# Performance work log

Hardware: AMD Instinct MI355X
Metric: run time of the kernel (lower is better)

## Reference

```python
import jax, jax.numpy as jnp
import numpy as np

N = 10000      # nodes
E = 100000     # edges
D = 768        # hidden = heads * head_dim
H = 4          # heads
C = D // H     # 192 per-head channels
EDIM = 16      # edge feature dim
NREL = 10      # num relations
L = 3          # num TransformerConv layers


def setup_inputs() -> dict:
    key = jax.random.key(0)
    ks = jax.random.split(key, 16)
    s = 0.02
    x = jax.random.normal(ks[0], (N, D), jnp.float32)
    edge_index = jax.random.randint(ks[1], (2, E), 0, N, jnp.int32)
    rel = jax.random.randint(ks[2], (E,), 0, NREL).astype(jnp.float32)
    w = jax.random.uniform(ks[3], (E,), jnp.float32)
    edge_attr = jnp.stack([rel, w], axis=1)  # [E, 2]: (relation_id, weight)
    rel_emb = jax.random.normal(ks[4], (NREL, EDIM - 1), jnp.float32) * s
    W_edge = jax.random.normal(ks[5], (EDIM, EDIM), jnp.float32) * s
    b_edge = jnp.zeros((EDIM,), jnp.float32)
    Wk = jax.random.normal(ks[6], (L, D, D), jnp.float32) * s
    bk = jnp.zeros((L, D), jnp.float32)
    Wq = jax.random.normal(ks[7], (L, D, D), jnp.float32) * s
    bq = jnp.zeros((L, D), jnp.float32)
    Wv = jax.random.normal(ks[8], (L, D, D), jnp.float32) * s
    bv = jnp.zeros((L, D), jnp.float32)
    We = jax.random.normal(ks[9], (L, EDIM, D), jnp.float32) * s   # lin_edge, no bias (PyG)
    Wskip = jax.random.normal(ks[10], (L, D, D), jnp.float32) * s  # root/skip linear
    bskip = jnp.zeros((L, D), jnp.float32)
    ln_g = jnp.ones((D,), jnp.float32)
    ln_b = jnp.zeros((D,), jnp.float32)
    return dict(x=x, edge_attr=edge_attr, edge_index=edge_index, rel_emb=rel_emb,
                W_edge=W_edge, b_edge=b_edge, Wk=Wk, bk=bk, Wq=Wq, bq=bq,
                Wv=Wv, bv=bv, We=We, Wskip=Wskip, bskip=bskip, ln_g=ln_g, ln_b=ln_b)


def reference(x, edge_attr, edge_index, rel_emb, W_edge, b_edge,
              Wk, bk, Wq, bq, Wv, bv, We, Wskip, bskip, ln_g, ln_b):
    src, dst = edge_index[0], edge_index[1]
    # _process_edge_features: embed relation id, concat weight, project
    rel_ids = jnp.clip(jax.lax.stop_gradient(edge_attr[:, 0]).astype(jnp.int32), 0, NREL - 1)
    ef = jnp.concatenate([rel_emb[rel_ids], edge_attr[:, 1:2]], axis=-1) @ W_edge + b_edge  # [E,16]
    scale = 1.0 / np.sqrt(C)
    h = x  # input_proj is Identity (input_dim == hidden_dim)
    for l in range(L):
        q = (h @ Wq[l] + bq[l]).reshape(N, H, C)
        k = (h @ Wk[l] + bk[l]).reshape(N, H, C)
        v = (h @ Wv[l] + bv[l]).reshape(N, H, C)
        e = (ef @ We[l]).reshape(E, H, C)           # per-edge embedding
        kj = k[src] + e                              # [E,H,C]
        alpha = jnp.einsum('ehc,ehc->eh', q[dst], kj) * scale  # [E,H]
        # scatter-softmax over incoming edges of each destination node
        m = jax.ops.segment_max(jax.lax.stop_gradient(alpha), dst, num_segments=N)
        a = jnp.exp(alpha - m[dst])
        denom = jax.ops.segment_sum(a, dst, num_segments=N)
        a = a / (denom[dst] + 1e-16)
        msg = (v[src] + e) * a[..., None]            # [E,H,C]
        out = jax.ops.segment_sum(msg.reshape(E, H * C), dst, num_segments=N)
        h = out + h @ Wskip[l] + bskip[l]            # root_weight skip connection
        if l < L - 1:
            h = jax.nn.gelu(h, approximate=False)    # dropout: eval mode -> identity
    mu = jnp.mean(h, axis=-1, keepdims=True)
    var = jnp.mean((h - mu) ** 2, axis=-1, keepdims=True)
    h = (h - mu) / jnp.sqrt(var + 1e-5) * ln_g + ln_b
    return jnp.mean(h, axis=0)  # global_mean_pool over single graph -> [D]
```

## Files before the change

### kernel.cpp

```cpp
#include <hip/hip_runtime.h>
#include <hip/hip_bf16.h>
#include <math.h>
#include <stdint.h>

#define NN 10000
#define EE 100000
#define DD 768
#define HH 4
#define CC 192
#define EDIM 16
#define NREL 10
#define MP 10240
#define NQ2 3200
#define NB 3136
#define SCALE 0.07216878364870322f

using short8  = __attribute__((ext_vector_type(8))) short;
using floatx4 = __attribute__((ext_vector_type(4))) float;


__device__ __forceinline__ float b2f(short u) {
    union { unsigned int i; float f; } t;
    t.i = ((unsigned int)(unsigned short)u) << 16;
    return t.f;
}

__device__ __forceinline__ short f2b(float f) {
    __hip_bfloat16 h = __float2bfloat16(f);
    short r;
    __builtin_memcpy(&r, &h, 2);
    return r;
}

__device__ __forceinline__ __hip_bfloat16 rd_any(const void* p, long long j, int bf) {
    if (bf) return ((const __hip_bfloat16*)p)[j];
    return __float2bfloat16(((const float*)p)[j]);
}

__device__ __forceinline__ void gload16(const __hip_bfloat16* g, __hip_bfloat16* l) {
    __builtin_amdgcn_global_load_lds(
        (const __attribute__((address_space(1))) unsigned int*)g,
        (__attribute__((address_space(3))) unsigned int*)l, 16, 0, 0);
}

__global__ __launch_bounds__(256) void detect_zero(const void* edge_attr,
                                                   int* flag, int* counts,
                                                   float* accum) {
    int i = blockIdx.x * 256 + threadIdx.x;
    if (i < NN) counts[i] = 0;
    if (i < DD) accum[i] = 0.0f;
    if (blockIdx.x == 0 && threadIdx.x < 64) {
        const unsigned short* p = (const unsigned short*)edge_attr;
        int nz = (p[4 * threadIdx.x] != 0) ? 1 : 0;
        unsigned long long m = __ballot(nz);
        if (threadIdx.x == 0) *flag = (__popcll(m) > 8) ? 1 : 0;
    }
}


__global__ __launch_bounds__(256) void cvt_big(
    const void* x, const void* We, const int* flag,
    __hip_bfloat16* hb, __hip_bfloat16* Web) {
    long long i = (long long)blockIdx.x * 256 + threadIdx.x;
    int bf = *flag;
    const long long NX = (long long)NN * DD;
    const long long NE2 = 3LL * EDIM * DD;
    if (i < NX) { hb[i] = rd_any(x, i, bf); return; } i -= NX;
    if (i < NE2) { Web[i] = rd_any(We, i, bf); return; } i -= NE2;
    if (i < (long long)(MP - NN) * DD) hb[(long long)NN * DD + i] = __float2bfloat16(0.0f);
}

__global__ __launch_bounds__(256) void cvt_small(
    const void* ea, const void* rel, const void* Wed, const void* bed,
    const void* bk, const void* bq, const void* bv, const void* bs,
    const void* lg, const void* lb, const int* flag,
    __hip_bfloat16* eab, __hip_bfloat16* relb, __hip_bfloat16* Wedb,
    __hip_bfloat16* bedb, __hip_bfloat16* ballb, __hip_bfloat16* lgb,
    __hip_bfloat16* lbb) {
    long long i = (long long)blockIdx.x * 256 + threadIdx.x;
    int bf = *flag;
    if (i < 2LL * EE) { eab[i] = rd_any(ea, i, bf); return; } i -= 2LL * EE;
    if (i < NREL * (EDIM - 1)) { relb[i] = rd_any(rel, i, bf); return; } i -= NREL * (EDIM - 1);
    if (i < EDIM * EDIM) { Wedb[i] = rd_any(Wed, i, bf); return; } i -= EDIM * EDIM;
    if (i < EDIM) { bedb[i] = rd_any(bed, i, bf); return; } i -= EDIM;
    if (i < 3 * NB) {
        int l = (int)(i / NB), c = (int)(i % NB);
        const void* src; long long off; int outc;
        if (c < 768)       { src = bq; off = (long long)l * DD + c; outc = c; }
        else if (c < 1536) { int xx = c - 768;  src = bk;
                             off = (long long)l * DD + xx;
                             outc = 768 + (xx / 6) * 12 + xx % 6; }
        else if (c < 2304) { int xx = c - 1536; src = bv;
                             off = (long long)l * DD + xx;
                             outc = 768 + (xx / 6) * 12 + 6 + xx % 6; }
        else if (c < 3072) { src = bs; off = (long long)l * DD + (c - 2304); outc = c; }
        else { ballb[l * NB + c] = __float2bfloat16(0.0f); return; }
        ballb[l * NB + outc] = rd_any(src, off, bf); return;
    } i -= 3 * NB;
    if (i < DD) { lgb[i] = rd_any(lg, i, bf); return; } i -= DD;
    if (i < DD) { lbb[i] = rd_any(lb, i, bf); return; }
}

__global__ __launch_bounds__(256) void wt_all(
    const void* Wq, const void* Wk, const void* Wv, const void* Ws,
    const int* flag, __hip_bfloat16* Wt3) {
    __shared__ __hip_bfloat16 tile[32][33];
    int mm = blockIdx.y;
    int l = mm >> 2, m = mm & 3;
    const void* src = (m == 0) ? Wq : (m == 1) ? Wk : (m == 2) ? Wv : Ws;
    int bx = blockIdx.x;
    int tr = bx / 24, tc = bx % 24;
    int k0 = tr * 32, c0 = tc * 32;
    int t = threadIdx.x;
    int rr = t >> 5, cc = t & 31;
    int bf = *flag;
    long long base = (long long)l * DD * DD;
#pragma unroll
    for (int p = 0; p < 4; p++)
        tile[p * 8 + rr][cc] =
            rd_any(src, base + (long long)(k0 + p * 8 + rr) * DD + c0 + cc, bf);
    __syncthreads();
    __hip_bfloat16* base_l = Wt3 + (size_t)l * NB * DD;
#pragma unroll
    for (int p = 0; p < 4; p++) {
        int xcol = c0 + p * 8 + rr;
        int row;
        if (m == 1)      row = 768 + (xcol / 6) * 12 + xcol % 6;
        else if (m == 2) row = 768 + (xcol / 6) * 12 + 6 + xcol % 6;
        else             row = m * 768 + xcol;
        base_l[(size_t)row * DD + k0 + cc] = tile[cc][p * 8 + rr];
    }
}

__global__ __launch_bounds__(256) void mq_kernel(
    const void* Wq, const void* bq, const int* flag,
    const __hip_bfloat16* __restrict__ Web, __hip_bfloat16* __restrict__ Wt3,
    __hip_bfloat16* __restrict__ ballb) {
    __shared__ float WeS[16][193];
    const int lh = blockIdx.y, l = lh >> 2, hh = lh & 3;
    const int t = threadIdx.x;
    const int bf = *flag;
    for (int i = t; i < 16 * 192; i += 256) {
        int j = i / 192, c = i % 192;
        WeS[j][c] = (float)Web[(size_t)l * EDIM * DD + (size_t)j * DD + hh * CC + c];
    }
    __syncthreads();
    const int k = blockIdx.x * 64 + (t >> 2);
    const int j0 = (t & 3) * 4;
    float s0 = 0.f, s1 = 0.f, s2 = 0.f, s3 = 0.f;
    if (bf) {
        const short8* qp = (const short8*)((const __hip_bfloat16*)Wq +
            ((size_t)l * DD + k) * DD + hh * CC);
#pragma unroll 4
        for (int ch = 0; ch < 24; ch++) {
            short8 v = qp[ch];
#pragma unroll
            for (int u = 0; u < 8; u++) {
                float w = b2f(v[u]);
                int c = ch * 8 + u;
                s0 += w * WeS[j0 + 0][c]; s1 += w * WeS[j0 + 1][c];
                s2 += w * WeS[j0 + 2][c]; s3 += w * WeS[j0 + 3][c];
            }
        }
    } else {
        const float4* qp = (const float4*)((const float*)Wq +
            ((size_t)l * DD + k) * DD + hh * CC);
#pragma unroll 4
        for (int ch = 0; ch < 48; ch++) {
            float4 v = qp[ch];
            float wv[4] = {v.x, v.y, v.z, v.w};
#pragma unroll
            for (int u = 0; u < 4; u++) {
                float w = wv[u];
                int c = ch * 4 + u;
                s0 += w * WeS[j0 + 0][c]; s1 += w * WeS[j0 + 1][c];
                s2 += w * WeS[j0 + 2][c]; s3 += w * WeS[j0 + 3][c];
            }
        }
    }
    const size_t base = (size_t)l * NB * DD;
    const int row = 3072 + hh * 16 + j0;
    Wt3[base + (size_t)(row + 0) * DD + k] = __float2bfloat16(s0);
    Wt3[base + (size_t)(row + 1) * DD + k] = __float2bfloat16(s1);
    Wt3[base + (size_t)(row + 2) * DD + k] = __float2bfloat16(s2);
    Wt3[base + (size_t)(row + 3) * DD + k] = __float2bfloat16(s3);
    if (blockIdx.x == 0 && t < 4) {
        float b0 = 0.f, b1 = 0.f, b2 = 0.f, b3 = 0.f;
        for (int c = 0; c < CC; c++) {
            float w = (float)rd_any(bq, (long long)l * DD + hh * CC + c, bf);
            b0 += w * WeS[j0 + 0][c]; b1 += w * WeS[j0 + 1][c];
            b2 += w * WeS[j0 + 2][c]; b3 += w * WeS[j0 + 3][c];
        }
        ballb[l * NB + 3072 + hh * 16 + j0 + 0] = __float2bfloat16(b0);
        ballb[l * NB + 3072 + hh * 16 + j0 + 1] = __float2bfloat16(b1);
        ballb[l * NB + 3072 + hh * 16 + j0 + 2] = __float2bfloat16(b2);
        ballb[l * NB + 3072 + hh * 16 + j0 + 3] = __float2bfloat16(b3);
    }
}


__global__ __launch_bounds__(256) void count_kernel(const int* ei, int* counts) {
    int e = blockIdx.x * 256 + threadIdx.x;
    if (e < EE) atomicAdd(&counts[ei[EE + e]], 1);
}

__global__ __launch_bounds__(256) void scan_kernel(const int* counts, int* rowptr,
                                                   int* cursor) {
    __shared__ int buf[NN];
    __shared__ int sdata[256];
    int t = threadIdx.x;
    for (int j = t; j < NN; j += 256) buf[j] = counts[j];
    __syncthreads();
    int base = t * 40;
    int cnt = (base < NN) ? min(40, NN - base) : 0;
    int s = 0;
    for (int i = 0; i < cnt; i++) s += buf[base + i];
    sdata[t] = s;
    __syncthreads();
    for (int off = 1; off < 256; off <<= 1) {
        int add = (t >= off) ? sdata[t - off] : 0;
        __syncthreads();
        sdata[t] += add;
        __syncthreads();
    }
    int run = sdata[t] - s;
    for (int i = 0; i < cnt; i++) {
        int tmp = buf[base + i];
        buf[base + i] = run;
        run += tmp;
    }
    __syncthreads();
    for (int j = t; j < NN; j += 256) {
        int v = buf[j];
        cursor[j] = v;
        rowptr[j] = v;
    }
    if (t == 0) rowptr[NN] = EE;
}

__global__ __launch_bounds__(256) void fill_kernel(const int* ei, int* cursor,
                                                   int* eids, int* esrc) {
    int e = blockIdx.x * 256 + threadIdx.x;
    if (e < EE) {
        int d = ei[EE + e];
        int pos = atomicAdd(&cursor[d], 1);
        eids[pos] = e;
        esrc[pos] = ei[e];
    }
}


__global__ __launch_bounds__(256) void ef_kernel(
    const int* __restrict__ eids,
    const __hip_bfloat16* __restrict__ eab, const __hip_bfloat16* __restrict__ relb,
    const __hip_bfloat16* __restrict__ Wedb, const __hip_bfloat16* __restrict__ bedb,
    __hip_bfloat16* __restrict__ efb) {
    int idx = blockIdx.x * 256 + threadIdx.x;
    if (idx >= EE * EDIM) return;
    int p = idx >> 4, j = idx & 15;
    int e = eids[p];
    int rid = (int)((float)eab[e * 2 + 0]);
    rid = min(max(rid, 0), NREL - 1);
    float w = (float)eab[e * 2 + 1];
    float s = (float)bedb[j];
#pragma unroll
    for (int i = 0; i < 15; i++)
        s += (float)relb[rid * 15 + i] * (float)Wedb[i * EDIM + j];
    s += w * (float)Wedb[15 * EDIM + j];
    efb[idx] = __float2bfloat16(s);
}


__device__ __forceinline__ void stage_half(const __hip_bfloat16* g, int row0, int ktile,
                                           char* ldsdst, int tid) {
#pragma unroll
    for (int j = 0; j < 2; ++j) {
        int c = j * 512 + tid;
        int row = c >> 3;
        int sch = (c & 7) ^ (row & 7);
        gload16(g + (size_t)(row0 + row) * DD + ktile * 64 + sch * 8,
                (__hip_bfloat16*)(ldsdst + c * 16));
    }
}

#define MF16(va, vb, cc) cc = __builtin_amdgcn_mfma_f32_16x16x32_bf16(va, vb, cc, 0, 0, 0)
#define BAR() __builtin_amdgcn_s_barrier()
#define WLG() asm volatile("s_waitcnt lgkmcnt(0)" ::: "memory")
#define WVM(N) asm volatile("s_waitcnt vmcnt(" #N ")" ::: "memory")
#define SB() __builtin_amdgcn_sched_barrier(0)
#define LDS8(off) (*(const short8*)(smem + (off)))

__global__ __launch_bounds__(512) void gemm256(
    const __hip_bfloat16* __restrict__ A, const __hip_bfloat16* __restrict__ Bt,
    const __hip_bfloat16* __restrict__ bias, __hip_bfloat16* __restrict__ C) {
    __shared__ __align__(16) char smem[131072];
    const int bid = (int)blockIdx.x;
    const int tid = threadIdx.x;
    const int wid = tid >> 6, lane = tid & 63;
    const int quad = lane >> 4, l15 = lane & 15;

    if (bid < 160) {
        const int m0q = bid * 64;
        const __hip_bfloat16* Bq = Bt + (size_t)3072 * DD;
        const int xq0 = (quad ^ (l15 & 7)) * 16;
        const int xq1 = ((quad + 4) ^ (l15 & 7)) * 16;
        floatx4 qacc[4] = {};
        for (int kt = 0; kt < 12; ++kt) {
#pragma unroll
            for (int j = 0; j < 2; ++j) {
                int c = j * 512 + tid;
                int hf = c >> 9;
                int cc = c & 511;
                int row = cc >> 3;
                int sch = (cc & 7) ^ (row & 7);
                const __hip_bfloat16* src = hf
                    ? (Bq + (size_t)row * DD + kt * 64 + sch * 8)
                    : (A + (size_t)(m0q + row) * DD + kt * 64 + sch * 8);
                gload16(src, (__hip_bfloat16*)(smem + c * 16));
            }
            asm volatile("s_waitcnt vmcnt(0)" ::: "memory");
            BAR();
            if (wid < 4) {
                short8 a0 = LDS8((wid * 16 + l15) * 128 + xq0);
                short8 a1 = LDS8((wid * 16 + l15) * 128 + xq1);
#pragma unroll
                for (int nt = 0; nt < 4; ++nt) {
                    short8 b0 = LDS8(8192 + (nt * 16 + l15) * 128 + xq0);
                    short8 b1 = LDS8(8192 + (nt * 16 + l15) * 128 + xq1);
                    MF16(a0, b0, qacc[nt]);
                    MF16(a1, b1, qacc[nt]);
                }
            }
            WLG();
            BAR();
        }
        if (wid < 4) {
#pragma unroll
            for (int nt = 0; nt < 4; ++nt) {
                float bb = (float)bias[3072 + nt * 16 + l15];
#pragma unroll
                for (int r = 0; r < 4; ++r) {
                    int row = m0q + wid * 16 + quad * 4 + r;
                    if (row < NN)
                        C[(size_t)row * NQ2 + 3072 + nt * 16 + l15] =
                            __float2bfloat16(qacc[nt][r] + bb);
                }
            }
        }
        return;
    }

    const int mbid = bid - 160;
    const int wm = wid >> 2, wn = wid & 3;
    const int swz = (mbid & 7) * 60 + (mbid >> 3);
    const int m0 = (swz / 12) * 256;
    const int n0 = (swz % 12) * 256;

    const int xa0 = (quad ^ (l15 & 7)) * 16;
    const int xa1 = ((quad + 4) ^ (l15 & 7)) * 16;
    const int aRow = (wm * 128 + l15) * 128;
    const int bRow = 32768 + (wn * 64 + l15) * 128;

    floatx4 acc[8][4] = {};
    short8 a[4][2], bA[2][2], bB[2][2];

    stage_half(A, m0, 0, smem + 0, tid);
    stage_half(A, m0 + 128, 0, smem + 16384, tid);
    stage_half(Bt, n0, 0, smem + 32768, tid);
    stage_half(Bt, n0 + 128, 0, smem + 49152, tid);
    stage_half(Bt, n0, 1, smem + 98304, tid);
    stage_half(Bt, n0 + 128, 1, smem + 114688, tid);
    WVM(4);
    BAR();

#pragma unroll 1
    for (int it = 0; it < 6; ++it) {
        const int kA = 2 * it + 1;
        const int kB = (it < 5) ? 2 * it + 2 : 0;
        const int kC = (it < 5) ? 2 * it + 3 : 1;
        stage_half(A, m0, kA, smem + 65536, tid);
        stage_half(A, m0 + 128, kA, smem + 81920, tid);
#pragma unroll
        for (int mt = 0; mt < 4; ++mt) {
            a[mt][0] = LDS8(aRow + mt * 2048 + xa0);
            a[mt][1] = LDS8(aRow + mt * 2048 + xa1);
        }
#pragma unroll
        for (int nt = 0; nt < 2; ++nt) {
            bA[nt][0] = LDS8(bRow + nt * 2048 + xa0);
            bA[nt][1] = LDS8(bRow + nt * 2048 + xa1);
            bB[nt][0] = LDS8(bRow + (nt + 2) * 2048 + xa0);
            bB[nt][1] = LDS8(bRow + (nt + 2) * 2048 + xa1);
        }
        SB(); BAR(); WLG(); SB();
        __builtin_amdgcn_s_setprio(1);
#pragma unroll
        for (int mt = 0; mt < 4; ++mt)
#pragma unroll
            for (int nt = 0; nt < 2; ++nt) {
                MF16(a[mt][0], bA[nt][0], acc[mt][nt]);
                MF16(a[mt][1], bA[nt][1], acc[mt][nt]);
                MF16(a[mt][0], bB[nt][0], acc[mt][nt + 2]);
                MF16(a[mt][1], bB[nt][1], acc[mt][nt + 2]);
            }
        __builtin_amdgcn_s_setprio(0);
        stage_half(Bt, n0, kB, smem + 32768, tid);
        stage_half(Bt, n0 + 128, kB, smem + 49152, tid);
#pragma unroll
        for (int mt = 0; mt < 4; ++mt) {
            a[mt][0] = LDS8(aRow + (mt + 4) * 2048 + xa0);
            a[mt][1] = LDS8(aRow + (mt + 4) * 2048 + xa1);
        }
        WVM(4);
        SB(); BAR(); WLG(); SB();
        __builtin_amdgcn_s_setprio(1);
#pragma unroll
        for (int mt = 0; mt < 4; ++mt)
#pragma unroll
            for (int nt = 0; nt < 2; ++nt) {
                MF16(a[mt][0], bB[nt][0], acc[mt + 4][nt + 2]);
                MF16(a[mt][1], bB[nt][1], acc[mt + 4][nt + 2]);
                MF16(a[mt][0], bA[nt][0], acc[mt + 4][nt]);
                MF16(a[mt][1], bA[nt][1], acc[mt + 4][nt]);
            }
        __builtin_amdgcn_s_setprio(0);
        stage_half(A, m0, kB, smem + 0, tid);
        stage_half(A, m0 + 128, kB, smem + 16384, tid);
#pragma unroll
        for (int mt = 0; mt < 4; ++mt) {
            a[mt][0] = LDS8(65536 + aRow + mt * 2048 + xa0);
            a[mt][1] = LDS8(65536 + aRow + mt * 2048 + xa1);
        }
#pragma unroll
        for (int nt = 0; nt < 2; ++nt) {
            bA[nt][0] = LDS8(65536 + bRow + nt * 2048 + xa0);
            bA[nt][1] = LDS8(65536 + bRow + nt * 2048 + xa1);
            bB[nt][0] = LDS8(65536 + bRow + (nt + 2) * 2048 + xa0);
            bB[nt][1] = LDS8(65536 + bRow + (nt + 2) * 2048 + xa1);
        }
        SB(); BAR(); WLG(); SB();
        __builtin_amdgcn_s_setprio(1);
#pragma unroll
        for (int mt = 0; mt < 4; ++mt)
#pragma unroll
            for (int nt = 0; nt < 2; ++nt) {
                MF16(a[mt][0], bA[nt][0], acc[mt][nt]);
                MF16(a[mt][1], bA[nt][1], acc[mt][nt]);
                MF16(a[mt][0], bB[nt][0], acc[mt][nt + 2]);
                MF16(a[mt][1], bB[nt][1], acc[mt][nt + 2]);
            }
        __builtin_amdgcn_s_setprio(0);
        stage_half(Bt, n0, kC, smem + 98304, tid);
        stage_half(Bt, n0 + 128, kC, smem + 114688, tid);
#pragma unroll
        for (int mt = 0; mt < 4; ++mt) {
            a[mt][0] = LDS8(65536 + aRow + (mt + 4) * 2048 + xa0);
            a[mt][1] = LDS8(65536 + aRow + (mt + 4) * 2048 + xa1);
        }
        WVM(4);
        SB(); BAR(); WLG(); SB();
        __builtin_amdgcn_s_setprio(1);
#pragma unroll
        for (int mt = 0; mt < 4; ++mt)
#pragma unroll
            for (int nt = 0; nt < 2; ++nt) {
                MF16(a[mt][0], bB[nt][0], acc[mt + 4][nt + 2]);
                MF16(a[mt][1], bB[nt][1], acc[mt + 4][nt + 2]);
                MF16(a[mt][0], bA[nt][0], acc[mt + 4][nt]);
                MF16(a[mt][1], bA[nt][1], acc[mt + 4][nt]);
            }
        __builtin_amdgcn_s_setprio(0);
    }

    asm volatile("s_waitcnt vmcnt(0)" ::: "memory");
    BAR();
    {
        short* stg = (short*)smem + wid * 1152;
        float bv[4];
#pragma unroll
        for (int nt = 0; nt < 4; ++nt)
            bv[nt] = (float)bias[n0 + wn * 64 + nt * 16 + l15];
        const int rdo = (lane >> 2) * 68 + (lane & 3) * 16;
        const int grow0 = m0 + wm * 128 + (lane >> 2);
        const int gcol = n0 + wn * 64 + (lane & 3) * 16;
#pragma unroll
        for (int mt = 0; mt < 8; ++mt) {
#pragma unroll
            for (int nt = 0; nt < 4; ++nt)
#pragma unroll
                for (int r = 0; r < 4; ++r)
                    stg[(quad * 4 + r) * 68 + nt * 16 + l15] =
                        f2b(acc[mt][nt][r] + bv[nt]);
            asm volatile("s_waitcnt lgkmcnt(0)" ::: "memory");
            short8 v0 = *(const short8*)(stg + rdo);
            short8 v1 = *(const short8*)(stg + rdo + 8);
            int grow = grow0 + mt * 16;
            if (grow < NN) {
                short8* dp = (short8*)(C + (size_t)grow * NQ2 + gcol);
                dp[0] = v0; dp[1] = v1;
            }
            asm volatile("s_waitcnt lgkmcnt(0)" ::: "memory");
        }
    }
}


__global__ __launch_bounds__(256) void node_attn(
    const int* __restrict__ rowptr, const int* __restrict__ esrc,
    const __hip_bfloat16* __restrict__ qkvs, const __hip_bfloat16* __restrict__ efb,
    const __hip_bfloat16* __restrict__ Wel, __hip_bfloat16* __restrict__ hb,
    int do_gelu) {
    const int wv = threadIdx.x >> 6, lane = threadIdx.x & 63;
    const int n = blockIdx.x * 2 + (wv >> 1);
    const int half = wv & 1;
    const int cb = half * 384 + lane * 6;
    const int g = half * 64 + lane;
    const int kvoff = 768 + g * 12;
    const int sj = lane & 15;
    const int hsel = lane & 32;
    const float qe_gate = ((lane & 16) == 0) ? 1.0f : 0.0f;
    const int s0 = rowptr[n], s1 = rowptr[n + 1];
    const short* qk = (const short*)qkvs;
    float q[6];
    {
        const short2* qp = (const short2*)(qk + (size_t)n * NQ2 + cb);
        short2 a = qp[0], b = qp[1], c = qp[2];
        q[0] = b2f(a.x) * SCALE; q[1] = b2f(a.y) * SCALE; q[2] = b2f(b.x) * SCALE;
        q[3] = b2f(b.y) * SCALE; q[4] = b2f(c.x) * SCALE; q[5] = b2f(c.y) * SCALE;
    }
    const float qe_l = b2f(qk[(size_t)n * NQ2 + 3072 + (half * 2 + (lane >> 5)) * 16 + sj])
                       * SCALE * qe_gate;
    float m = -INFINITY, lsum = 0.f, sacc = 0.f;
    float acc[6] = {};
    short4 kvA = {0,0,0,0}, kvB = {0,0,0,0}, kvC = {0,0,0,0};
    float efv = 0.f;
    if (s0 < s1) {
        const short4* kv = (const short4*)(qk + (size_t)esrc[s0] * NQ2 + kvoff);
        kvA = kv[0]; kvB = kv[1]; kvC = kv[2];
        efv = b2f(((const short*)efb)[(size_t)s0 * 16 + sj]);
    }
    for (int p = s0; p < s1; p++) {
        short4 nA = kvA, nB = kvB, nC = kvC;
        float nefv = efv;
        if (p + 1 < s1) {
            const short4* kv = (const short4*)(qk + (size_t)esrc[p + 1] * NQ2 + kvoff);
            nA = kv[0]; nB = kv[1]; nC = kv[2];
            nefv = b2f(((const short*)efb)[(size_t)(p + 1) * 16 + sj]);
        }
        float part = qe_l * efv;
        part += q[0] * b2f(kvA.x) + q[1] * b2f(kvA.y) + q[2] * b2f(kvA.z);
        part += q[3] * b2f(kvA.w) + q[4] * b2f(kvB.x) + q[5] * b2f(kvB.y);
        part += __shfl_xor(part, 1); part += __shfl_xor(part, 2);
        part += __shfl_xor(part, 4); part += __shfl_xor(part, 8);
        part += __shfl_xor(part, 16);
        if (part > m + 8.0f) {
            float sc = __expf(m - part);
            m = part;
            lsum *= sc; sacc *= sc;
#pragma unroll
            for (int i = 0; i < 6; i++) acc[i] *= sc;
        }
        float w = __expf(part - m);
        lsum += w;
        sacc += w * efv;
        acc[0] += w * b2f(kvB.z); acc[1] += w * b2f(kvB.w);
        acc[2] += w * b2f(kvC.x); acc[3] += w * b2f(kvC.y);
        acc[4] += w * b2f(kvC.z); acc[5] += w * b2f(kvC.w);
        kvA = nA; kvB = nB; kvC = nC; efv = nefv;
    }
    float inv = 1.0f / (lsum + 1e-16f);
#pragma unroll
    for (int i = 0; i < 6; i++) acc[i] *= inv;
    float sS = sacc * inv;
    {
        const short2* sp = (const short2*)(qk + (size_t)n * NQ2 + 2304 + cb);
        short2 a = sp[0], b = sp[1], c = sp[2];
        acc[0] += b2f(a.x); acc[1] += b2f(a.y); acc[2] += b2f(b.x);
        acc[3] += b2f(b.y); acc[4] += b2f(c.x); acc[5] += b2f(c.y);
    }
#pragma unroll
    for (int j = 0; j < 16; j++) {
        float sv = __shfl(sS, hsel + j);
        const short2* wp = (const short2*)(Wel + (size_t)j * DD + cb);
        short2 a = wp[0], b = wp[1], c = wp[2];
        acc[0] += sv * b2f(a.x); acc[1] += sv * b2f(a.y); acc[2] += sv * b2f(b.x);
        acc[3] += sv * b2f(b.y); acc[4] += sv * b2f(c.x); acc[5] += sv * b2f(c.y);
    }
    if (do_gelu) {
#pragma unroll
        for (int i = 0; i < 6; i++)
            acc[i] = 0.5f * acc[i] * (1.0f + erff(acc[i] * 0.70710678118654752f));
    }
    short2 o0, o1, o2;
    o0.x = f2b(acc[0]); o0.y = f2b(acc[1]);
    o1.x = f2b(acc[2]); o1.y = f2b(acc[3]);
    o2.x = f2b(acc[4]); o2.y = f2b(acc[5]);
    short2* hp = (short2*)(hb + (size_t)n * DD + cb);
    hp[0] = o0; hp[1] = o1; hp[2] = o2;
}


__global__ __launch_bounds__(256) void ln_pool(
    const __hip_bfloat16* __restrict__ hb, const __hip_bfloat16* __restrict__ g,
    const __hip_bfloat16* __restrict__ b, float* __restrict__ accum) {
    __shared__ float sbuf[4][768];
    int grp = blockIdx.x, t = threadIdx.x;
    int wid = t >> 6, lane = t & 63;
    float gv[12], bv[12], acc[12];
#pragma unroll
    for (int i = 0; i < 12; i++) {
        gv[i] = (float)g[lane + i * 64];
        bv[i] = (float)b[lane + i * 64];
        acc[i] = 0.f;
    }
    for (int r = wid; r < 25; r += 4) {
        const __hip_bfloat16* row = hb + (size_t)(grp * 25 + r) * DD;
        float x[12];
        float s = 0.f, q = 0.f;
#pragma unroll
        for (int i = 0; i < 12; i++) {
            x[i] = (float)row[lane + i * 64];
            s += x[i]; q += x[i] * x[i];
        }
#pragma unroll
        for (int m = 32; m > 0; m >>= 1) {
            s += __shfl_xor(s, m); q += __shfl_xor(q, m);
        }
        float mu = s * (1.0f / 768.0f);
        float ms = q * (1.0f / 768.0f);
        float inv = 1.0f / sqrtf(ms - mu * mu + 1e-5f);
#pragma unroll
        for (int i = 0; i < 12; i++)
            acc[i] += (x[i] - mu) * inv * gv[i] + bv[i];
    }
#pragma unroll
    for (int i = 0; i < 12; i++) sbuf[wid][lane + i * 64] = acc[i];
    __syncthreads();
#pragma unroll
    for (int j = 0; j < 3; j++) {
        int col = t + j * 256;
        atomicAdd(&accum[col],
                  sbuf[0][col] + sbuf[1][col] + sbuf[2][col] + sbuf[3][col]);
    }
}

__global__ __launch_bounds__(256) void pool_final(
    const float* __restrict__ accum, void* __restrict__ out,
    const int* __restrict__ flag) {
    int dd = blockIdx.x * 256 + threadIdx.x;
    if (dd >= DD) return;
    float s = accum[dd] * (1.0f / 10000.0f);
    if (*flag) ((__hip_bfloat16*)out)[dd] = __float2bfloat16(s);
    else ((float*)out)[dd] = s;
}


extern "C" void kernel_launch(void* const* d_in, const int* in_sizes, int n_in,
                              void* d_out, int out_size, void* d_ws, size_t ws_size,
                              hipStream_t stream) {
    const void* x         = d_in[0];
    const void* edge_attr = d_in[1];
    const int*  ei        = (const int*)d_in[2];
    const void* rel_emb   = d_in[3];
    const void* W_edge    = d_in[4];
    const void* b_edge    = d_in[5];
    const void* Wk        = d_in[6];
    const void* bk        = d_in[7];
    const void* Wq        = d_in[8];
    const void* bq        = d_in[9];
    const void* Wv        = d_in[10];
    const void* bv        = d_in[11];
    const void* We        = d_in[12];
    const void* Wskip     = d_in[13];
    const void* bskip     = d_in[14];
    const void* ln_g      = d_in[15];
    const void* ln_b      = d_in[16];

    char* ws = (char*)d_ws;
    int*   flag    = (int*)(ws + 0);
    int*   counts  = (int*)(ws + 256);
    int*   rowptr  = (int*)(ws + 40448);
    int*   cursor  = (int*)(ws + 80640);
    int*   eids    = (int*)(ws + 120832);
    int*   esrc    = (int*)(ws + 520960);
    __hip_bfloat16* efb = (__hip_bfloat16*)(ws + 920960);
    float* accum   = (float*)(ws + 4120960);
    __hip_bfloat16* eab   = (__hip_bfloat16*)(ws + 5349760);
    __hip_bfloat16* relb  = (__hip_bfloat16*)(ws + 5749760);
    __hip_bfloat16* Wedb  = (__hip_bfloat16*)(ws + 5750144);
    __hip_bfloat16* bedb  = (__hip_bfloat16*)(ws + 5750656);
    __hip_bfloat16* ballb = (__hip_bfloat16*)(ws + 5750784);
    __hip_bfloat16* lngb  = (__hip_bfloat16*)(ws + 5770752);
    __hip_bfloat16* lnbb  = (__hip_bfloat16*)(ws + 5772288);
    __hip_bfloat16* Web   = (__hip_bfloat16*)(ws + 5773824);
    __hip_bfloat16* hb    = (__hip_bfloat16*)(ws + 5847552);
    __hip_bfloat16* Wt3   = (__hip_bfloat16*)(ws + 21576192);
    __hip_bfloat16* qkvs  = (__hip_bfloat16*)(ws + 36911616);

    dim3 blk(256);

    detect_zero<<<dim3(40), blk, 0, stream>>>(edge_attr, flag, counts, accum);

    {
        long long tot = (long long)NN * DD + 3LL * EDIM * DD + (long long)(MP - NN) * DD;
        cvt_big<<<dim3((unsigned)((tot + 255) / 256)), blk, 0, stream>>>(x, We, flag, hb, Web);
    }
    {
        long long tot = 2LL * EE + NREL * (EDIM - 1) + EDIM * EDIM + EDIM
                        + 3LL * NB + 2LL * DD;
        cvt_small<<<dim3((unsigned)((tot + 255) / 256)), blk, 0, stream>>>(
            edge_attr, rel_emb, W_edge, b_edge, bk, bq, bv, bskip, ln_g, ln_b,
            flag, eab, relb, Wedb, bedb, ballb, lngb, lnbb);
    }
    wt_all<<<dim3(576, 12), blk, 0, stream>>>(Wq, Wk, Wv, Wskip, flag, Wt3);
    mq_kernel<<<dim3(12, 12), blk, 0, stream>>>(Wq, bq, flag, Web, Wt3, ballb);

    count_kernel<<<dim3((EE + 255) / 256), blk, 0, stream>>>(ei, counts);
    scan_kernel<<<dim3(1), blk, 0, stream>>>(counts, rowptr, cursor);
    fill_kernel<<<dim3((EE + 255) / 256), blk, 0, stream>>>(ei, cursor, eids, esrc);

    ef_kernel<<<dim3((EE * EDIM) / 256), blk, 0, stream>>>(eids, eab, relb, Wedb, bedb, efb);

    for (int l = 0; l < 3; l++) {
        const __hip_bfloat16* We_l = Web + (size_t)l * EDIM * DD;
        gemm256<<<dim3(640), dim3(512), 0, stream>>>(
            hb, Wt3 + (size_t)l * NB * DD, ballb + (size_t)l * NB, qkvs);
        node_attn<<<dim3(NN / 2), blk, 0, stream>>>(rowptr, esrc, qkvs, efb,
                                                    We_l, hb, (l < 2) ? 1 : 0);
    }

    ln_pool<<<dim3(400), blk, 0, stream>>>(hb, lngb, lnbb, accum);
    pool_final<<<dim3(3), blk, 0, stream>>>(accum, d_out, flag);
}
```

Before: 570.9 us.

## Fuse setup kernels, sort nodes by degree, and fold pooling finalize into ln_pool

Removes the detect_zero and pool_final launches by recomputing the dtype flag inline in each kernel and finalizing the pooled output in the last ln_pool block via an atomic done counter. Fuses the edge-fill and edge-feature kernels into one pass that writes each edge's 16 features with vector stores. The scan now builds a descending-degree node order that node_attn uses to schedule high-degree nodes first for load balance. It also reorders gemm256 blocks so the small Q-projection blocks run last. The changes trade a few redundant flag reads and a fence for fewer launches and better tail balance, but atomic ordering makes the edge order within each node nondeterministic.

```diff
diff --git a/kernel.cpp b/kernel.cpp
--- a/kernel.cpp
+++ b/kernel.cpp
@@ -37,32 +37,30 @@
     return __float2bfloat16(((const float*)p)[j]);
 }
 
+__device__ __forceinline__ int detect_bf(const void* ea) {
+    const unsigned short* p = (const unsigned short*)ea;
+    int lane = threadIdx.x & 63;
+    int nz = (p[4 * lane] != 0) ? 1 : 0;
+    unsigned long long m = __ballot(nz);
+    return (__popcll(m) > 8) ? 1 : 0;
+}
+
 __device__ __forceinline__ void gload16(const __hip_bfloat16* g, __hip_bfloat16* l) {
     __builtin_amdgcn_global_load_lds(
         (const __attribute__((address_space(1))) unsigned int*)g,
         (__attribute__((address_space(3))) unsigned int*)l, 16, 0, 0);
 }
 
-__global__ __launch_bounds__(256) void detect_zero(const void* edge_attr,
-                                                   int* flag, int* counts,
-                                                   float* accum) {
-    int i = blockIdx.x * 256 + threadIdx.x;
+
+__global__ __launch_bounds__(256) void cvt_big(
+    const void* x, const void* We, const void* ea,
+    __hip_bfloat16* hb, __hip_bfloat16* Web,
+    int* counts, float* accum, int* done) {
+    long long i = (long long)blockIdx.x * 256 + threadIdx.x;
+    int bf = detect_bf(ea);
     if (i < NN) counts[i] = 0;
-    if (i < DD) accum[i] = 0.0f;
-    if (blockIdx.x == 0 && threadIdx.x < 64) {
-        const unsigned short* p = (const unsigned short*)edge_attr;
-        int nz = (p[4 * threadIdx.x] != 0) ? 1 : 0;
-        unsigned long long m = __ballot(nz);
-        if (threadIdx.x == 0) *flag = (__popcll(m) > 8) ? 1 : 0;
-    }
-}
-
-
-__global__ __launch_bounds__(256) void cvt_big(
-    const void* x, const void* We, const int* flag,
-    __hip_bfloat16* hb, __hip_bfloat16* Web) {
-    long long i = (long long)blockIdx.x * 256 + threadIdx.x;
-    int bf = *flag;
+    if (i < DD) accum[(int)i] = 0.0f;
+    if (i == 0) *done = 0;
     const long long NX = (long long)NN * DD;
     const long long NE2 = 3LL * EDIM * DD;
     if (i < NX) { hb[i] = rd_any(x, i, bf); return; } i -= NX;
@@ -73,12 +71,12 @@
 __global__ __launch_bounds__(256) void cvt_small(
     const void* ea, const void* rel, const void* Wed, const void* bed,
     const void* bk, const void* bq, const void* bv, const void* bs,
-    const void* lg, const void* lb, const int* flag,
+    const void* lg, const void* lb,
     __hip_bfloat16* eab, __hip_bfloat16* relb, __hip_bfloat16* Wedb,
     __hip_bfloat16* bedb, __hip_bfloat16* ballb, __hip_bfloat16* lgb,
     __hip_bfloat16* lbb) {
     long long i = (long long)blockIdx.x * 256 + threadIdx.x;
-    int bf = *flag;
+    int bf = detect_bf(ea);
     if (i < 2LL * EE) { eab[i] = rd_any(ea, i, bf); return; } i -= 2LL * EE;
     if (i < NREL * (EDIM - 1)) { relb[i] = rd_any(rel, i, bf); return; } i -= NREL * (EDIM - 1);
     if (i < EDIM * EDIM) { Wedb[i] = rd_any(Wed, i, bf); return; } i -= EDIM * EDIM;
@@ -103,8 +101,9 @@
 
 __global__ __launch_bounds__(256) void wt_all(
     const void* Wq, const void* Wk, const void* Wv, const void* Ws,
-    const int* flag, __hip_bfloat16* Wt3) {
+    const void* ea, __hip_bfloat16* Wt3) {
     __shared__ __hip_bfloat16 tile[32][33];
+    int bf = detect_bf(ea);
     int mm = blockIdx.y;
     int l = mm >> 2, m = mm & 3;
     const void* src = (m == 0) ? Wq : (m == 1) ? Wk : (m == 2) ? Wv : Ws;
@@ -113,7 +112,6 @@
     int k0 = tr * 32, c0 = tc * 32;
     int t = threadIdx.x;
     int rr = t >> 5, cc = t & 31;
-    int bf = *flag;
     long long base = (long long)l * DD * DD;
 #pragma unroll
     for (int p = 0; p < 4; p++)
@@ -133,13 +131,13 @@
 }
 
 __global__ __launch_bounds__(256) void mq_kernel(
-    const void* Wq, const void* bq, const int* flag,
+    const void* Wq, const void* bq, const void* ea,
     const __hip_bfloat16* __restrict__ Web, __hip_bfloat16* __restrict__ Wt3,
     __hip_bfloat16* __restrict__ ballb) {
     __shared__ float WeS[16][193];
+    const int bf = detect_bf(ea);
     const int lh = blockIdx.y, l = lh >> 2, hh = lh & 3;
     const int t = threadIdx.x;
-    const int bf = *flag;
     for (int i = t; i < 16 * 192; i += 256) {
         int j = i / 192, c = i % 192;
         WeS[j][c] = (float)Web[(size_t)l * EDIM * DD + (size_t)j * DD + hh * CC + c];
@@ -205,18 +203,29 @@
 }
 
 __global__ __launch_bounds__(256) void scan_kernel(const int* counts, int* rowptr,
-                                                   int* cursor) {
+                                                   int* cursor, int* order) {
     __shared__ int buf[NN];
     __shared__ int sdata[256];
+    __shared__ int hist[64];
+    __shared__ int hcur[64];
     int t = threadIdx.x;
+    if (t < 64) hist[t] = 0;
     for (int j = t; j < NN; j += 256) buf[j] = counts[j];
     __syncthreads();
     int base = t * 40;
     int cnt = (base < NN) ? min(40, NN - base) : 0;
     int s = 0;
-    for (int i = 0; i < cnt; i++) s += buf[base + i];
+    for (int i = 0; i < cnt; i++) {
+        int d = buf[base + i];
+        s += d;
+        atomicAdd(&hist[min(d, 63)], 1);
+    }
     sdata[t] = s;
     __syncthreads();
+    if (t == 0) {
+        int run = 0;
+        for (int d = 63; d >= 0; --d) { hcur[d] = run; run += hist[d]; }
+    }
     for (int off = 1; off < 256; off <<= 1) {
         int add = (t >= off) ? sdata[t - off] : 0;
         __syncthreads();
@@ -225,49 +234,48 @@
     }
     int run = sdata[t] - s;
     for (int i = 0; i < cnt; i++) {
-        int tmp = buf[base + i];
-        buf[base + i] = run;
-        run += tmp;
-    }
-    __syncthreads();
-    for (int j = t; j < NN; j += 256) {
-        int v = buf[j];
-        cursor[j] = v;
-        rowptr[j] = v;
+        int d = buf[base + i];
+        int pos = atomicAdd(&hcur[min(d, 63)], 1);
+        order[pos] = base + i;
+        cursor[base + i] = run;
+        rowptr[base + i] = run;
+        run += d;
     }
     if (t == 0) rowptr[NN] = EE;
 }
 
-__global__ __launch_bounds__(256) void fill_kernel(const int* ei, int* cursor,
-                                                   int* eids, int* esrc) {
-    int e = blockIdx.x * 256 + threadIdx.x;
-    if (e < EE) {
-        int d = ei[EE + e];
-        int pos = atomicAdd(&cursor[d], 1);
-        eids[pos] = e;
-        esrc[pos] = ei[e];
-    }
-}
-
-
-__global__ __launch_bounds__(256) void ef_kernel(
-    const int* __restrict__ eids,
+__global__ __launch_bounds__(256) void fill_ef(
+    const int* __restrict__ ei, int* __restrict__ cursor, int* __restrict__ esrc,
     const __hip_bfloat16* __restrict__ eab, const __hip_bfloat16* __restrict__ relb,
     const __hip_bfloat16* __restrict__ Wedb, const __hip_bfloat16* __restrict__ bedb,
     __hip_bfloat16* __restrict__ efb) {
-    int idx = blockIdx.x * 256 + threadIdx.x;
-    if (idx >= EE * EDIM) return;
-    int p = idx >> 4, j = idx & 15;
-    int e = eids[p];
+    __shared__ float WedS[16][17];
+    __shared__ float relS[NREL][15];
+    __shared__ float bedS[16];
+    int t = threadIdx.x;
+    if (t < 256) WedS[t >> 4][t & 15] = (float)Wedb[t];
+    if (t < NREL * 15) relS[t / 15][t % 15] = (float)relb[t];
+    if (t < 16) bedS[t] = (float)bedb[t];
+    __syncthreads();
+    int e = blockIdx.x * 256 + t;
+    if (e >= EE) return;
+    int d = ei[EE + e];
+    int pos = atomicAdd(&cursor[d], 1);
+    esrc[pos] = ei[e];
     int rid = (int)((float)eab[e * 2 + 0]);
     rid = min(max(rid, 0), NREL - 1);
     float w = (float)eab[e * 2 + 1];
-    float s = (float)bedb[j];
-#pragma unroll
-    for (int i = 0; i < 15; i++)
-        s += (float)relb[rid * 15 + i] * (float)Wedb[i * EDIM + j];
-    s += w * (float)Wedb[15 * EDIM + j];
-    efb[idx] = __float2bfloat16(s);
+    short8 o0, o1;
+#pragma unroll
+    for (int j = 0; j < 16; j++) {
+        float s = bedS[j];
+#pragma unroll
+        for (int i = 0; i < 15; i++) s += relS[rid][i] * WedS[i][j];
+        s += w * WedS[15][j];
+        if (j < 8) o0[j] = f2b(s); else o1[j - 8] = f2b(s);
+    }
+    *(short8*)(efb + (size_t)pos * 16) = o0;
+    *(short8*)(efb + (size_t)pos * 16 + 8) = o1;
 }
 
 
@@ -299,8 +307,8 @@
     const int wid = tid >> 6, lane = tid & 63;
     const int quad = lane >> 4, l15 = lane & 15;
 
-    if (bid < 160) {
-        const int m0q = bid * 64;
+    if (bid >= 480) {
+        const int m0q = (bid - 480) * 64;
         const __hip_bfloat16* Bq = Bt + (size_t)3072 * DD;
         const int xq0 = (quad ^ (l15 & 7)) * 16;
         const int xq1 = ((quad + 4) ^ (l15 & 7)) * 16;
@@ -350,9 +358,8 @@
         return;
     }
 
-    const int mbid = bid - 160;
     const int wm = wid >> 2, wn = wid & 3;
-    const int swz = (mbid & 7) * 60 + (mbid >> 3);
+    const int swz = (bid & 7) * 60 + (bid >> 3);
     const int m0 = (swz / 12) * 256;
     const int n0 = (swz % 12) * 256;
 
@@ -507,11 +514,12 @@
 
 __global__ __launch_bounds__(256) void node_attn(
     const int* __restrict__ rowptr, const int* __restrict__ esrc,
+    const int* __restrict__ order,
     const __hip_bfloat16* __restrict__ qkvs, const __hip_bfloat16* __restrict__ efb,
     const __hip_bfloat16* __restrict__ Wel, __hip_bfloat16* __restrict__ hb,
     int do_gelu) {
     const int wv = threadIdx.x >> 6, lane = threadIdx.x & 63;
-    const int n = blockIdx.x * 2 + (wv >> 1);
+    const int n = order[blockIdx.x * 2 + (wv >> 1)];
     const int half = wv & 1;
     const int cb = half * 384 + lane * 6;
     const int g = half * 64 + lane;
@@ -602,8 +610,10 @@
 
 __global__ __launch_bounds__(256) void ln_pool(
     const __hip_bfloat16* __restrict__ hb, const __hip_bfloat16* __restrict__ g,
-    const __hip_bfloat16* __restrict__ b, float* __restrict__ accum) {
+    const __hip_bfloat16* __restrict__ b, float* __restrict__ accum,
+    int* __restrict__ done, const void* ea, void* __restrict__ out) {
     __shared__ float sbuf[4][768];
+    __shared__ int lastFlag;
     int grp = blockIdx.x, t = threadIdx.x;
     int wid = t >> 6, lane = t & 63;
     float gv[12], bv[12], acc[12];
@@ -642,16 +652,18 @@
         atomicAdd(&accum[col],
                   sbuf[0][col] + sbuf[1][col] + sbuf[2][col] + sbuf[3][col]);
     }
-}
-
-__global__ __launch_bounds__(256) void pool_final(
-    const float* __restrict__ accum, void* __restrict__ out,
-    const int* __restrict__ flag) {
-    int dd = blockIdx.x * 256 + threadIdx.x;
-    if (dd >= DD) return;
-    float s = accum[dd] * (1.0f / 10000.0f);
-    if (*flag) ((__hip_bfloat16*)out)[dd] = __float2bfloat16(s);
-    else ((float*)out)[dd] = s;
+    __threadfence();
+    if (t == 0) lastFlag = (atomicAdd(done, 1) == 399);
+    __syncthreads();
+    if (lastFlag) {
+        int bf = detect_bf(ea);
+        for (int j = t; j < DD; j += 256) {
+            float s = __hip_atomic_load(&accum[j], __ATOMIC_RELAXED,
+                                        __HIP_MEMORY_SCOPE_AGENT) * (1.0f / 10000.0f);
+            if (bf) ((__hip_bfloat16*)out)[j] = __float2bfloat16(s);
+            else ((float*)out)[j] = s;
+        }
+    }
 }
 
 
@@ -677,11 +689,11 @@
     const void* ln_b      = d_in[16];
 
     char* ws = (char*)d_ws;
-    int*   flag    = (int*)(ws + 0);
+    int*   done    = (int*)(ws + 0);
     int*   counts  = (int*)(ws + 256);
     int*   rowptr  = (int*)(ws + 40448);
     int*   cursor  = (int*)(ws + 80640);
-    int*   eids    = (int*)(ws + 120832);
+    int*   order   = (int*)(ws + 120832);
     int*   esrc    = (int*)(ws + 520960);
     __hip_bfloat16* efb = (__hip_bfloat16*)(ws + 920960);
     float* accum   = (float*)(ws + 4120960);
@@ -699,36 +711,34 @@
 
     dim3 blk(256);
 
-    detect_zero<<<dim3(40), blk, 0, stream>>>(edge_attr, flag, counts, accum);
-
     {
         long long tot = (long long)NN * DD + 3LL * EDIM * DD + (long long)(MP - NN) * DD;
-        cvt_big<<<dim3((unsigned)((tot + 255) / 256)), blk, 0, stream>>>(x, We, flag, hb, Web);
+        cvt_big<<<dim3((unsigned)((tot + 255) / 256)), blk, 0, stream>>>(
+            x, We, edge_attr, hb, Web, counts, accum, done);
     }
     {
         long long tot = 2LL * EE + NREL * (EDIM - 1) + EDIM * EDIM + EDIM
                         + 3LL * NB + 2LL * DD;
         cvt_small<<<dim3((unsigned)((tot + 255) / 256)), blk, 0, stream>>>(
             edge_attr, rel_emb, W_edge, b_edge, bk, bq, bv, bskip, ln_g, ln_b,
-            flag, eab, relb, Wedb, bedb, ballb, lngb, lnbb);
-    }
-    wt_all<<<dim3(576, 12), blk, 0, stream>>>(Wq, Wk, Wv, Wskip, flag, Wt3);
-    mq_kernel<<<dim3(12, 12), blk, 0, stream>>>(Wq, bq, flag, Web, Wt3, ballb);
+            eab, relb, Wedb, bedb, ballb, lngb, lnbb);
+    }
+    wt_all<<<dim3(576, 12), blk, 0, stream>>>(Wq, Wk, Wv, Wskip, edge_attr, Wt3);
+    mq_kernel<<<dim3(12, 12), blk, 0, stream>>>(Wq, bq, edge_attr, Web, Wt3, ballb);
 
     count_kernel<<<dim3((EE + 255) / 256), blk, 0, stream>>>(ei, counts);
-    scan_kernel<<<dim3(1), blk, 0, stream>>>(counts, rowptr, cursor);
-    fill_kernel<<<dim3((EE + 255) / 256), blk, 0, stream>>>(ei, cursor, eids, esrc);
-
-    ef_kernel<<<dim3((EE * EDIM) / 256), blk, 0, stream>>>(eids, eab, relb, Wedb, bedb, efb);
+    scan_kernel<<<dim3(1), blk, 0, stream>>>(counts, rowptr, cursor, order);
+    fill_ef<<<dim3((EE + 255) / 256), blk, 0, stream>>>(
+        ei, cursor, esrc, eab, relb, Wedb, bedb, efb);
 
     for (int l = 0; l < 3; l++) {
         const __hip_bfloat16* We_l = Web + (size_t)l * EDIM * DD;
         gemm256<<<dim3(640), dim3(512), 0, stream>>>(
             hb, Wt3 + (size_t)l * NB * DD, ballb + (size_t)l * NB, qkvs);
-        node_attn<<<dim3(NN / 2), blk, 0, stream>>>(rowptr, esrc, qkvs, efb,
+        node_attn<<<dim3(NN / 2), blk, 0, stream>>>(rowptr, esrc, order, qkvs, efb,
                                                     We_l, hb, (l < 2) ? 1 : 0);
     }
 
-    ln_pool<<<dim3(400), blk, 0, stream>>>(hb, lngb, lnbb, accum);
-    pool_final<<<dim3(3), blk, 0, stream>>>(accum, d_out, flag);
-}
+    ln_pool<<<dim3(400), blk, 0, stream>>>(hb, lngb, lnbb, accum, done,
+                                           edge_attr, d_out);
+}
```

Result: no change. 581.4 us (+1.8%).
